# Kernel optimization log

Hardware: AMD Instinct MI355X
Metric: run time of the kernel (lower is better)

Reference implementation:

```python
import jax, jax.numpy as jnp
import numpy as np

IN_FEATURES = 8192
OUT_FEATURES = 8192
BITS = 4
TILE = 16
M_TOKENS = 64  # small token count -> dequant-traffic dominated (memory regime)
SCALE_BLOCK = 128


def setup_inputs() -> dict:
    key = jax.random.key(0)
    k1, k2, k3, k4, k5, k6 = jax.random.split(key, 6)
    tiles_k = IN_FEATURES // TILE
    tiles_n = OUT_FEATURES // TILE
    packed_bytes = 256 * BITS // 8  # 128 bytes per 16x16 tile for 4-bit
    x = jax.random.normal(k1, (M_TOKENS, IN_FEATURES), dtype=jnp.float32)
    packed_indices = jax.random.randint(k2, (tiles_k, tiles_n, packed_bytes), 0, 256, dtype=jnp.int32)
    scales = jax.random.uniform(k3, ((IN_FEATURES + SCALE_BLOCK - 1) // SCALE_BLOCK, OUT_FEATURES), dtype=jnp.float32, minval=0.5, maxval=1.5)
    su = jax.random.normal(k4, (IN_FEATURES,), dtype=jnp.float32)
    sv = jax.random.normal(k5, (OUT_FEATURES,), dtype=jnp.float32)
    grid = jax.random.normal(k6, (2 ** BITS,), dtype=jnp.float32)  # trellis codebook grid
    return {"x": x, "packed_indices": packed_indices, "scales": scales, "su": su, "sv": sv, "grid": grid}


def _dequantize(packed_indices, scales, su, sv, grid):
    # packed_indices: [tiles_k, tiles_n, packed_bytes] byte values (0..255)
    tk, tn, pb = packed_indices.shape
    bits = (pb * 8) // (TILE * TILE)
    # unpack bytes -> bits (little-endian within byte), then group into bits-per-index
    bitplane = (packed_indices[..., None] >> jnp.arange(8, dtype=jnp.int32)) & 1  # [tk, tn, pb, 8]
    idx = (bitplane.reshape(tk, tn, TILE * TILE, bits)
           * (2 ** jnp.arange(bits, dtype=jnp.int32))).sum(-1)  # [tk, tn, 256]
    vals = grid[idx].reshape(tk, tn, TILE, TILE)  # tile element order: (k_in_tile, n_in_tile)
    # assemble full weight laid out [K_in, N_out]
    W = vals.transpose(0, 2, 1, 3).reshape(tk * TILE, tn * TILE)
    # per-128-row-block scales over the K dim
    nb = scales.shape[0]
    W = (W.reshape(nb, SCALE_BLOCK, tn * TILE) * scales[:, None, :]).reshape(tk * TILE, tn * TILE)
    # per-row (su) and per-column (sv) scale/sign vectors
    W = W * su[:, None] * sv[None, :]
    return W  # [in_features, out_features]


def reference(x, packed_indices, scales, su, sv, grid):
    W = _dequantize(packed_indices, scales, su, sv, grid)  # [K, N]
    # torch: x.view(-1, K) @ weights[N, K].T  ==  x @ W[K, N]
    lead = x.shape[:-1]
    out = x.reshape(-1, W.shape[0]) @ W
    return out.reshape(*lead, W.shape[1])
```

## Files before the change

### kernel.cpp

```cpp
#include <hip/hip_runtime.h>

typedef float f32x4 __attribute__((ext_vector_type(4)));
typedef __bf16 bf16x8 __attribute__((ext_vector_type(8)));

#define K_FEAT 8192
#define N_FEAT 8192
#define M_TOK 64
#define TILES_N 512
#define TILES_K 512
#define WROWSTRIDE 40

__device__ __forceinline__ unsigned short f2bf(float f) {
    unsigned int u = __builtin_bit_cast(unsigned int, f);
    u = (u + 0x7FFFu + ((u >> 16) & 1u)) >> 16;
    return (unsigned short)u;
}

__global__ void __launch_bounds__(256)
prep_x_kernel(const float* __restrict__ x, const float* __restrict__ su,
              unsigned short* __restrict__ xb)
{
    int i = blockIdx.x * 256 + threadIdx.x;
    const float4* x4 = (const float4*)x;
    const float4* su4 = (const float4*)su;
    float4 xv = x4[i];
    float4 s4 = su4[i & (K_FEAT / 4 - 1)];
    ushort4 o;
    o.x = f2bf(xv.x * s4.x);
    o.y = f2bf(xv.y * s4.y);
    o.z = f2bf(xv.z * s4.z);
    o.w = f2bf(xv.w * s4.w);
    ((ushort4*)xb)[i] = o;
}

__global__ void __launch_bounds__(256)
trellis_main(const int* __restrict__ packed,
             const float* __restrict__ scales,
             const float* __restrict__ sv,
             const float* __restrict__ grid,
             const unsigned short* __restrict__ xb,
             float* __restrict__ partials,
             int lg_ksplit)
{
    __shared__ unsigned int table[256];
    __shared__ unsigned short wlds[2][64 * WROWSTRIDE];

    const int tid = threadIdx.x;
    const int bid = blockIdx.x;
    const int ksplit = 1 << lg_ksplit;
    const int s = bid & (ksplit - 1);
    const int ng = bid >> lg_ksplit;
    const int col0 = ng * 64;
    const int nt0 = ng * 4;
    const int ktile0 = s * (TILES_K >> lg_ksplit);
    const int nstep = (TILES_K >> lg_ksplit) >> 1;

    const int tau = tid >> 5;
    const int dkt = tau >> 2;
    const int dnt_s = tau & 3;
    const int w = tid & 31;
    const int c = w & 7;
    const int g = w >> 3;

    const int* pb = packed
        + ((size_t)(ktile0 + dkt) * TILES_N + (nt0 + dnt_s)) * 128 + c + 32 * g;
    const int stepstride = 2 * TILES_N * 128;

    const int wave = tid >> 6;
    const int lane = tid & 63;
    const int ln15 = lane & 15;
    const int kgrp = (lane >> 4) * 8;
    const unsigned short* xrow = xb + (size_t)(wave * 16 + ln15) * K_FEAT;

    {
        float lo = grid[tid & 15];
        float hi = grid[(tid >> 4) & 15];
        table[tid] = (unsigned int)f2bf(lo) | ((unsigned int)f2bf(hi) << 16);
    }

    int ld0 = pb[0], ld1 = pb[8], ld2 = pb[16], ld3 = pb[24];
    uint4 ra = *(const uint4*)(xrow + ktile0 * 16 + kgrp);

    f32x4 acc[4], acc2[4];
    for (int d = 0; d < 4; ++d)
        for (int j = 0; j < 4; ++j) { acc[d][j] = 0.f; acc2[d][j] = 0.f; }

    __syncthreads();

    for (int t = 0; t < nstep; ++t) {
        const int* pn = pb + (size_t)(t + 1 < nstep ? (t + 1) : 0) * stepstride;
        int n0 = pn[0], n1 = pn[8], n2 = pn[16], n3 = pn[24];

        unsigned int t0 = table[ld0 & 255];
        unsigned int t1 = table[ld1 & 255];
        unsigned int t2 = table[ld2 & 255];
        unsigned int t3 = table[ld3 & 255];
        unsigned int w0 = (t0 & 0xFFFFu) | (t1 << 16);
        unsigned int w1 = (t2 & 0xFFFFu) | (t3 << 16);
        unsigned int w2 = (t0 >> 16)     | (t1 & 0xFFFF0000u);
        unsigned int w3 = (t2 >> 16)     | (t3 & 0xFFFF0000u);
        {
            int nrow = dnt_s * 16 + 2 * c;
            int koff = dkt * 16 + 4 * g;
            unsigned short* dst = &wlds[t & 1][nrow * WROWSTRIDE + koff];
            *(uint2*)dst = make_uint2(w0, w1);
            *(uint2*)(dst + WROWSTRIDE) = make_uint2(w2, w3);
        }

        __syncthreads();

        int k0n = ktile0 * 16 + (t + 1 < nstep ? (t + 1) : 0) * 32;
        uint4 ran = *(const uint4*)(xrow + k0n + kgrp);

        bf16x8 a = __builtin_bit_cast(bf16x8, ra);
        const unsigned short* wbase = &wlds[t & 1][0];
        for (int d = 0; d < 4; ++d) {
            bf16x8 b = *(const bf16x8*)(wbase + (d * 16 + ln15) * WROWSTRIDE + kgrp);
            acc2[d] = __builtin_amdgcn_mfma_f32_16x16x32_bf16(a, b, acc2[d], 0, 0, 0);
        }
        ra = ran;
        ld0 = n0; ld1 = n1; ld2 = n2; ld3 = n3;

        if ((t & 3) == 3) {
            int kb = (ktile0 * 16 + (t & ~3) * 32) >> 7;
            const float* srow = scales + (size_t)kb * N_FEAT + col0 + ln15;
            for (int d = 0; d < 4; ++d) {
                float sc = srow[d * 16];
                acc[d] += acc2[d] * sc;
                for (int j = 0; j < 4; ++j) acc2[d][j] = 0.f;
            }
        }
    }

    float* pout = partials + (size_t)s * (M_TOK * N_FEAT);
    const int rbase = (lane >> 4) * 4;
    for (int d = 0; d < 4; ++d) {
        int n = col0 + d * 16 + ln15;
        float svv = sv[n];
        for (int j = 0; j < 4; ++j) {
            int m = wave * 16 + rbase + j;
            pout[(size_t)m * N_FEAT + n] = acc[d][j] * svv;
        }
    }
}

__global__ void __launch_bounds__(256)
reduce_kernel(const float* __restrict__ partials, float* __restrict__ out, int ksplit)
{
    int i = blockIdx.x * 256 + threadIdx.x;
    const float4* p4 = (const float4*)partials;
    float4 a = p4[i];
    for (int k = 1; k < ksplit; ++k) {
        float4 v = p4[(size_t)k * (M_TOK * N_FEAT / 4) + i];
        a.x += v.x; a.y += v.y; a.z += v.z; a.w += v.w;
    }
    ((float4*)out)[i] = a;
}

extern "C" void kernel_launch(void* const* d_in, const int* in_sizes, int n_in,
                              void* d_out, int out_size, void* d_ws, size_t ws_size,
                              hipStream_t stream)
{
    const float* x      = (const float*)d_in[0];
    const int*   packed = (const int*)d_in[1];
    const float* scales = (const float*)d_in[2];
    const float* su     = (const float*)d_in[3];
    const float* sv     = (const float*)d_in[4];
    const float* grid   = (const float*)d_in[5];
    float* out = (float*)d_out;

    unsigned short* xb = (unsigned short*)d_ws;
    const size_t xb_bytes = (size_t)M_TOK * K_FEAT * 2;
    int lg = 3;
    while (lg > 0 &&
           xb_bytes + ((size_t)(1 << lg)) * M_TOK * N_FEAT * 4 > ws_size) --lg;
    const int ksplit = 1 << lg;
    float* partials = (float*)((char*)d_ws + xb_bytes);

    prep_x_kernel<<<(M_TOK * K_FEAT / 4) / 256, 256, 0, stream>>>(x, su, xb);
    trellis_main<<<(N_FEAT / 64) * ksplit, 256, 0, stream>>>(
        packed, scales, sv, grid, xb, partials, lg);
    reduce_kernel<<<(M_TOK * N_FEAT / 4) / 256, 256, 0, stream>>>(partials, out, ksplit);
}
```

Measured before the change: 42.36 us.

## Reshape block tile to 32 columns by 64 K, deepen prefetch, halve k-split

After: 57.71 us. 36.2% more time.

```diff
diff --git a/kernel.cpp b/kernel.cpp
--- a/kernel.cpp
+++ b/kernel.cpp
@@ -8,7 +8,7 @@
 #define M_TOK 64
 #define TILES_N 512
 #define TILES_K 512
-#define WROWSTRIDE 40
+#define WSTR 72
 
 __device__ __forceinline__ unsigned short f2bf(float f) {
     unsigned int u = __builtin_bit_cast(unsigned int, f);
@@ -43,34 +43,35 @@
              int lg_ksplit)
 {
     __shared__ unsigned int table[256];
-    __shared__ unsigned short wlds[2][64 * WROWSTRIDE];
+    __shared__ unsigned short wlds[2][32 * WSTR];
 
     const int tid = threadIdx.x;
     const int bid = blockIdx.x;
     const int ksplit = 1 << lg_ksplit;
     const int s = bid & (ksplit - 1);
     const int ng = bid >> lg_ksplit;
-    const int col0 = ng * 64;
-    const int nt0 = ng * 4;
+    const int col0 = ng * 32;
+    const int nt0 = ng * 2;
     const int ktile0 = s * (TILES_K >> lg_ksplit);
-    const int nstep = (TILES_K >> lg_ksplit) >> 1;
+    const int nstep = (TILES_K >> lg_ksplit) >> 2;
 
     const int tau = tid >> 5;
-    const int dkt = tau >> 2;
-    const int dnt_s = tau & 3;
+    const int dkt = tau >> 1;
+    const int dnt = tau & 1;
     const int w = tid & 31;
     const int c = w & 7;
     const int g = w >> 3;
 
     const int* pb = packed
-        + ((size_t)(ktile0 + dkt) * TILES_N + (nt0 + dnt_s)) * 128 + c + 32 * g;
-    const int stepstride = 2 * TILES_N * 128;
+        + ((size_t)(ktile0 + dkt) * TILES_N + (nt0 + dnt)) * 128 + c + 32 * g;
+    const long stepstride = 4L * TILES_N * 128;
 
     const int wave = tid >> 6;
     const int lane = tid & 63;
     const int ln15 = lane & 15;
     const int kgrp = (lane >> 4) * 8;
-    const unsigned short* xrow = xb + (size_t)(wave * 16 + ln15) * K_FEAT;
+    const unsigned short* xrow = xb + (size_t)(wave * 16 + ln15) * K_FEAT
+                                    + ktile0 * 16 + kgrp;
 
     {
         float lo = grid[tid & 15];
@@ -78,53 +79,65 @@
         table[tid] = (unsigned int)f2bf(lo) | ((unsigned int)f2bf(hi) << 16);
     }
 
-    int ld0 = pb[0], ld1 = pb[8], ld2 = pb[16], ld3 = pb[24];
-    uint4 ra = *(const uint4*)(xrow + ktile0 * 16 + kgrp);
+    int a0 = pb[0], a1 = pb[8], a2 = pb[16], a3 = pb[24];
+    const int* p1 = pb + stepstride;
+    int b0 = p1[0], b1 = p1[8], b2 = p1[16], b3 = p1[24];
 
-    f32x4 acc[4], acc2[4];
-    for (int d = 0; d < 4; ++d)
+    uint4 ra0 = *(const uint4*)(xrow);
+    uint4 ra1 = *(const uint4*)(xrow + 32);
+
+    f32x4 acc[2], acc2[2];
+    for (int d = 0; d < 2; ++d)
         for (int j = 0; j < 4; ++j) { acc[d][j] = 0.f; acc2[d][j] = 0.f; }
 
     __syncthreads();
 
     for (int t = 0; t < nstep; ++t) {
-        const int* pn = pb + (size_t)(t + 1 < nstep ? (t + 1) : 0) * stepstride;
-        int n0 = pn[0], n1 = pn[8], n2 = pn[16], n3 = pn[24];
+        int c0, c1, c2, c3;
+        if (t + 2 < nstep) {
+            const int* pn = pb + stepstride * (t + 2);
+            c0 = pn[0]; c1 = pn[8]; c2 = pn[16]; c3 = pn[24];
+        } else { c0 = c1 = c2 = c3 = 0; }
 
-        unsigned int t0 = table[ld0 & 255];
-        unsigned int t1 = table[ld1 & 255];
-        unsigned int t2 = table[ld2 & 255];
-        unsigned int t3 = table[ld3 & 255];
+        unsigned int t0 = table[a0 & 255];
+        unsigned int t1 = table[a1 & 255];
+        unsigned int t2 = table[a2 & 255];
+        unsigned int t3 = table[a3 & 255];
         unsigned int w0 = (t0 & 0xFFFFu) | (t1 << 16);
         unsigned int w1 = (t2 & 0xFFFFu) | (t3 << 16);
         unsigned int w2 = (t0 >> 16)     | (t1 & 0xFFFF0000u);
         unsigned int w3 = (t2 >> 16)     | (t3 & 0xFFFF0000u);
         {
-            int nrow = dnt_s * 16 + 2 * c;
-            int koff = dkt * 16 + 4 * g;
-            unsigned short* dst = &wlds[t & 1][nrow * WROWSTRIDE + koff];
+            unsigned short* dst =
+                &wlds[t & 1][(dnt * 16 + 2 * c) * WSTR + dkt * 16 + 4 * g];
             *(uint2*)dst = make_uint2(w0, w1);
-            *(uint2*)(dst + WROWSTRIDE) = make_uint2(w2, w3);
+            *(uint2*)(dst + WSTR) = make_uint2(w2, w3);
         }
 
         __syncthreads();
 
-        int k0n = ktile0 * 16 + (t + 1 < nstep ? (t + 1) : 0) * 32;
-        uint4 ran = *(const uint4*)(xrow + k0n + kgrp);
+        const unsigned short* xn = xrow + (t + 1 < nstep ? t + 1 : 0) * 64;
+        uint4 rn0 = *(const uint4*)(xn);
+        uint4 rn1 = *(const uint4*)(xn + 32);
 
-        bf16x8 a = __builtin_bit_cast(bf16x8, ra);
-        const unsigned short* wbase = &wlds[t & 1][0];
-        for (int d = 0; d < 4; ++d) {
-            bf16x8 b = *(const bf16x8*)(wbase + (d * 16 + ln15) * WROWSTRIDE + kgrp);
-            acc2[d] = __builtin_amdgcn_mfma_f32_16x16x32_bf16(a, b, acc2[d], 0, 0, 0);
+        bf16x8 aa0 = __builtin_bit_cast(bf16x8, ra0);
+        bf16x8 aa1 = __builtin_bit_cast(bf16x8, ra1);
+        const unsigned short* wb = &wlds[t & 1][0];
+        for (int d = 0; d < 2; ++d) {
+            const unsigned short* br = wb + (d * 16 + ln15) * WSTR + kgrp;
+            bf16x8 b0f = *(const bf16x8*)(br);
+            acc2[d] = __builtin_amdgcn_mfma_f32_16x16x32_bf16(aa0, b0f, acc2[d], 0, 0, 0);
+            bf16x8 b1f = *(const bf16x8*)(br + 32);
+            acc2[d] = __builtin_amdgcn_mfma_f32_16x16x32_bf16(aa1, b1f, acc2[d], 0, 0, 0);
         }
-        ra = ran;
-        ld0 = n0; ld1 = n1; ld2 = n2; ld3 = n3;
+        ra0 = rn0; ra1 = rn1;
+        a0 = b0; a1 = b1; a2 = b2; a3 = b3;
+        b0 = c0; b1 = c1; b2 = c2; b3 = c3;
 
-        if ((t & 3) == 3) {
-            int kb = (ktile0 * 16 + (t & ~3) * 32) >> 7;
+        if (t & 1) {
+            int kb = (ktile0 >> 3) + (t >> 1);
             const float* srow = scales + (size_t)kb * N_FEAT + col0 + ln15;
-            for (int d = 0; d < 4; ++d) {
+            for (int d = 0; d < 2; ++d) {
                 float sc = srow[d * 16];
                 acc[d] += acc2[d] * sc;
                 for (int j = 0; j < 4; ++j) acc2[d][j] = 0.f;
@@ -134,7 +147,7 @@
 
     float* pout = partials + (size_t)s * (M_TOK * N_FEAT);
     const int rbase = (lane >> 4) * 4;
-    for (int d = 0; d < 4; ++d) {
+    for (int d = 0; d < 2; ++d) {
         int n = col0 + d * 16 + ln15;
         float svv = sv[n];
         for (int j = 0; j < 4; ++j) {
@@ -171,14 +184,14 @@
 
     unsigned short* xb = (unsigned short*)d_ws;
     const size_t xb_bytes = (size_t)M_TOK * K_FEAT * 2;
-    int lg = 3;
+    int lg = 2;
     while (lg > 0 &&
            xb_bytes + ((size_t)(1 << lg)) * M_TOK * N_FEAT * 4 > ws_size) --lg;
     const int ksplit = 1 << lg;
     float* partials = (float*)((char*)d_ws + xb_bytes);
 
     prep_x_kernel<<<(M_TOK * K_FEAT / 4) / 256, 256, 0, stream>>>(x, su, xb);
-    trellis_main<<<(N_FEAT / 64) * ksplit, 256, 0, stream>>>(
+    trellis_main<<<(N_FEAT / 32) * ksplit, 256, 0, stream>>>(
         packed, scales, sv, grid, xb, partials, lg);
     reduce_kernel<<<(M_TOK * N_FEAT / 4) / 256, 256, 0, stream>>>(partials, out, ksplit);
 }
```

## Store split-K partials in bf16 and stage scales in LDS

Applied to the files above, without the earlier changes.

Result: faster. 38.04 us (-10.2%).

```diff
diff --git a/kernel.cpp b/kernel.cpp
--- a/kernel.cpp
+++ b/kernel.cpp
@@ -9,11 +9,17 @@
 #define TILES_N 512
 #define TILES_K 512
 #define WROWSTRIDE 40
+#define LG_KSPLIT 3
+#define KSPLIT 8
+#define NSTEP 32
 
 __device__ __forceinline__ unsigned short f2bf(float f) {
     unsigned int u = __builtin_bit_cast(unsigned int, f);
     u = (u + 0x7FFFu + ((u >> 16) & 1u)) >> 16;
     return (unsigned short)u;
+}
+__device__ __forceinline__ float bf2f(unsigned short h) {
+    return __builtin_bit_cast(float, (unsigned int)h << 16);
 }
 
 __global__ void __launch_bounds__(256)
@@ -39,21 +45,19 @@
              const float* __restrict__ sv,
              const float* __restrict__ grid,
              const unsigned short* __restrict__ xb,
-             float* __restrict__ partials,
-             int lg_ksplit)
+             unsigned short* __restrict__ partials)
 {
     __shared__ unsigned int table[256];
     __shared__ unsigned short wlds[2][64 * WROWSTRIDE];
+    __shared__ float slds[8 * 64];
 
     const int tid = threadIdx.x;
     const int bid = blockIdx.x;
-    const int ksplit = 1 << lg_ksplit;
-    const int s = bid & (ksplit - 1);
-    const int ng = bid >> lg_ksplit;
+    const int s = bid & (KSPLIT - 1);
+    const int ng = bid >> LG_KSPLIT;
     const int col0 = ng * 64;
     const int nt0 = ng * 4;
-    const int ktile0 = s * (TILES_K >> lg_ksplit);
-    const int nstep = (TILES_K >> lg_ksplit) >> 1;
+    const int ktile0 = s * (TILES_K / KSPLIT);
 
     const int tau = tid >> 5;
     const int dkt = tau >> 2;
@@ -77,6 +81,11 @@
         float hi = grid[(tid >> 4) & 15];
         table[tid] = (unsigned int)f2bf(lo) | ((unsigned int)f2bf(hi) << 16);
     }
+    {
+        const int kb0 = s * 8;
+        slds[tid]       = scales[(size_t)(kb0 + (tid >> 6)) * N_FEAT + col0 + (tid & 63)];
+        slds[tid + 256] = scales[(size_t)(kb0 + 4 + (tid >> 6)) * N_FEAT + col0 + (tid & 63)];
+    }
 
     int ld0 = pb[0], ld1 = pb[8], ld2 = pb[16], ld3 = pb[24];
     uint4 ra = *(const uint4*)(xrow + ktile0 * 16 + kgrp);
@@ -87,9 +96,12 @@
 
     __syncthreads();
 
-    for (int t = 0; t < nstep; ++t) {
-        const int* pn = pb + (size_t)(t + 1 < nstep ? (t + 1) : 0) * stepstride;
-        int n0 = pn[0], n1 = pn[8], n2 = pn[16], n3 = pn[24];
+    for (int t = 0; t < NSTEP; ++t) {
+        int n0 = 0, n1 = 0, n2 = 0, n3 = 0;
+        if (t + 1 < NSTEP) {
+            const int* pn = pb + (size_t)(t + 1) * stepstride;
+            n0 = pn[0]; n1 = pn[8]; n2 = pn[16]; n3 = pn[24];
+        }
 
         unsigned int t0 = table[ld0 & 255];
         unsigned int t1 = table[ld1 & 255];
@@ -107,9 +119,12 @@
             *(uint2*)(dst + WROWSTRIDE) = make_uint2(w2, w3);
         }
 
-        __syncthreads();
-
-        int k0n = ktile0 * 16 + (t + 1 < nstep ? (t + 1) : 0) * 32;
+        __builtin_amdgcn_sched_barrier(0);
+        asm volatile("s_waitcnt lgkmcnt(0)" ::: "memory");
+        __builtin_amdgcn_s_barrier();
+        __builtin_amdgcn_sched_barrier(0);
+
+        int k0n = ktile0 * 16 + (t + 1 < NSTEP ? (t + 1) : 0) * 32;
         uint4 ran = *(const uint4*)(xrow + k0n + kgrp);
 
         bf16x8 a = __builtin_bit_cast(bf16x8, ra);
@@ -122,8 +137,7 @@
         ld0 = n0; ld1 = n1; ld2 = n2; ld3 = n3;
 
         if ((t & 3) == 3) {
-            int kb = (ktile0 * 16 + (t & ~3) * 32) >> 7;
-            const float* srow = scales + (size_t)kb * N_FEAT + col0 + ln15;
+            const float* srow = slds + (t >> 2) * 64 + ln15;
             for (int d = 0; d < 4; ++d) {
                 float sc = srow[d * 16];
                 acc[d] += acc2[d] * sc;
@@ -132,29 +146,37 @@
         }
     }
 
-    float* pout = partials + (size_t)s * (M_TOK * N_FEAT);
+    unsigned short* pout = partials + (size_t)s * (M_TOK * N_FEAT);
     const int rbase = (lane >> 4) * 4;
     for (int d = 0; d < 4; ++d) {
         int n = col0 + d * 16 + ln15;
         float svv = sv[n];
         for (int j = 0; j < 4; ++j) {
             int m = wave * 16 + rbase + j;
-            pout[(size_t)m * N_FEAT + n] = acc[d][j] * svv;
+            pout[(size_t)m * N_FEAT + n] = f2bf(acc[d][j] * svv);
         }
     }
 }
 
 __global__ void __launch_bounds__(256)
-reduce_kernel(const float* __restrict__ partials, float* __restrict__ out, int ksplit)
+reduce_kernel(const unsigned short* __restrict__ partials, float* __restrict__ out)
 {
     int i = blockIdx.x * 256 + threadIdx.x;
-    const float4* p4 = (const float4*)partials;
-    float4 a = p4[i];
-    for (int k = 1; k < ksplit; ++k) {
-        float4 v = p4[(size_t)k * (M_TOK * N_FEAT / 4) + i];
-        a.x += v.x; a.y += v.y; a.z += v.z; a.w += v.w;
-    }
-    ((float4*)out)[i] = a;
+    const uint4* p = (const uint4*)partials;
+    float acc[8];
+    for (int e = 0; e < 8; ++e) acc[e] = 0.f;
+    for (int k = 0; k < KSPLIT; ++k) {
+        uint4 v = p[(size_t)k * (M_TOK * N_FEAT / 8) + i];
+        unsigned int uu[4] = {v.x, v.y, v.z, v.w};
+        for (int q = 0; q < 4; ++q) {
+            acc[2 * q]     += bf2f((unsigned short)(uu[q] & 0xFFFFu));
+            acc[2 * q + 1] += bf2f((unsigned short)(uu[q] >> 16));
+        }
+    }
+    float4 o0 = make_float4(acc[0], acc[1], acc[2], acc[3]);
+    float4 o1 = make_float4(acc[4], acc[5], acc[6], acc[7]);
+    ((float4*)out)[2 * i]     = o0;
+    ((float4*)out)[2 * i + 1] = o1;
 }
 
 extern "C" void kernel_launch(void* const* d_in, const int* in_sizes, int n_in,
@@ -171,14 +193,10 @@
 
     unsigned short* xb = (unsigned short*)d_ws;
     const size_t xb_bytes = (size_t)M_TOK * K_FEAT * 2;
-    int lg = 3;
-    while (lg > 0 &&
-           xb_bytes + ((size_t)(1 << lg)) * M_TOK * N_FEAT * 4 > ws_size) --lg;
-    const int ksplit = 1 << lg;
-    float* partials = (float*)((char*)d_ws + xb_bytes);
+    unsigned short* partials = (unsigned short*)((char*)d_ws + xb_bytes);
 
     prep_x_kernel<<<(M_TOK * K_FEAT / 4) / 256, 256, 0, stream>>>(x, su, xb);
-    trellis_main<<<(N_FEAT / 64) * ksplit, 256, 0, stream>>>(
-        packed, scales, sv, grid, xb, partials, lg);
-    reduce_kernel<<<(M_TOK * N_FEAT / 4) / 256, 256, 0, stream>>>(partials, out, ksplit);
-}
+    trellis_main<<<(N_FEAT / 64) * KSPLIT, 256, 0, stream>>>(
+        packed, scales, sv, grid, xb, partials);
+    reduce_kernel<<<(M_TOK * N_FEAT / 8) / 256, 256, 0, stream>>>(partials, out);
+}
```
